# Performance work log

Measured on AMD Instinct MI355X. Metric: run time of the kernel, lower is better.

## Reference

```python
import jax, jax.numpy as jnp
import numpy as np

N_NODES = 100000
N_EDGES = 1600000
NEG_SLOPE = 0.2  # DGL GATConv default leaky_relu slope
BN_EPS = 1e-5


def setup_inputs() -> dict:
    key = jax.random.key(0)
    ks = jax.random.split(key, 10)
    feats = jax.random.normal(ks[0], (N_NODES, 128), dtype=jnp.float32)
    src = jax.random.randint(ks[1], (N_EDGES,), 0, N_NODES, dtype=jnp.int64)
    dst = jax.random.randint(ks[2], (N_EDGES,), 0, N_NODES, dtype=jnp.int64)
    fc_w = jax.random.normal(ks[3], (256, 128), dtype=jnp.float32) * 0.05   # H*D x in_feats
    attn_l = jax.random.normal(ks[4], (4, 64), dtype=jnp.float32) * 0.05
    attn_r = jax.random.normal(ks[5], (4, 64), dtype=jnp.float32) * 0.05
    res_w = jax.random.normal(ks[6], (256, 128), dtype=jnp.float32) * 0.05  # residual projection
    bias = jax.random.normal(ks[7], (4, 64), dtype=jnp.float32) * 0.05
    gamma = jnp.ones((64,), dtype=jnp.float32)
    beta = jnp.zeros((64,), dtype=jnp.float32)
    return {"feats": feats, "src": src, "dst": dst, "fc_w": fc_w,
            "attn_l": attn_l, "attn_r": attn_r, "res_w": res_w,
            "bias": bias, "gamma": gamma, "beta": beta}


def reference(feats, src, dst, fc_w, attn_l, attn_r, res_w, bias, gamma, beta):
    N = feats.shape[0]
    H, D = attn_l.shape
    # projected features [N, H, D] (feat_drop is identity in eval mode)
    h = (feats @ fc_w.T).reshape(N, H, D)
    # per-node attention logits [N, H]
    el = jnp.sum(h * attn_l[None], axis=-1)
    er = jnp.sum(h * attn_r[None], axis=-1)
    # edge logits, leaky relu
    e = el[src] + er[dst]                       # [E, H]
    e = jnp.where(e > 0, e, NEG_SLOPE * e)
    # numerically stable segment softmax over incoming edges of each dst node
    m = jax.ops.segment_max(e, dst, num_segments=N)       # [N, H]
    ex = jnp.exp(e - m[dst])                               # [E, H]
    s = jax.ops.segment_sum(ex, dst, num_segments=N)       # [N, H]
    alpha = ex / s[dst]                                    # [E, H]
    # weighted message aggregation: scatter-add alpha * h_src into dst
    msg = h[src] * alpha[:, :, None]                       # [E, H, D]
    rst = jax.ops.segment_sum(msg, dst, num_segments=N)    # [N, H, D]
    # residual projection + bias + activation (elu)
    res = (feats @ res_w.T).reshape(N, H, D)
    rst = jax.nn.elu(rst + res + bias[None])
    # mean over heads -> [N, D]
    out = rst.mean(axis=1)
    # BatchNorm1d (training stats: biased variance over the node/batch axis)
    mu = out.mean(axis=0)
    var = out.var(axis=0)
    return (out - mu) * jax.lax.rsqrt(var + BN_EPS) * gamma + beta
```

## Files before the change

### kernel.cpp

```cpp
#include <hip/hip_runtime.h>

#define N_NODES 100000
#define N_PAD   100096
#define N_EDGES 1600000
#define NEG_SLOPE 0.2f
#define BN_EPS 1e-5f

typedef __attribute__((ext_vector_type(8))) short short8;
typedef __attribute__((ext_vector_type(4))) float floatx4;

static const size_t OFF_AB   = 0;
static const size_t OFF_BB   = 25624576;
static const size_t OFF_H    = 25755648;
static const size_t OFF_RES  = 76955648;
static const size_t OFF_EL   = 128155648;
static const size_t OFF_ER   = 129755648;
static const size_t OFF_DEG  = 131355648;
static const size_t OFF_RS   = 131755648;
static const size_t OFF_CUR  = 132155664;
static const size_t OFF_ESRC = 132555664;
static const size_t OFF_BS   = 138955664;
static const size_t OFF_BN   = 138956176;

__device__ __forceinline__ unsigned short f2bf(float x) {
  unsigned int u = __float_as_uint(x);
  unsigned int r = (u + 0x7fffu + ((u >> 16) & 1u)) >> 16;
  return (unsigned short)r;
}
__device__ __forceinline__ float bf2f(unsigned short u) {
  return __uint_as_float(((unsigned int)u) << 16);
}

__global__ __launch_bounds__(256) void k_pre(
    const float* __restrict__ feats, const float* __restrict__ fc_w,
    const float* __restrict__ res_w, const int* __restrict__ dst,
    unsigned short* __restrict__ Ab, unsigned short* __restrict__ Bb,
    int* __restrict__ deg)
{
  const int b = blockIdx.x;
  if (b < 6256) {
    int c = b * 256 + threadIdx.x;
    int r = c >> 4, j = c & 15;
    unsigned short v[8];
    if (r < N_NODES) {
      const float* p = feats + (size_t)r * 128 + j * 8;
      float4 a = *(const float4*)p, bb = *(const float4*)(p + 4);
      v[0]=f2bf(a.x); v[1]=f2bf(a.y); v[2]=f2bf(a.z); v[3]=f2bf(a.w);
      v[4]=f2bf(bb.x); v[5]=f2bf(bb.y); v[6]=f2bf(bb.z); v[7]=f2bf(bb.w);
    } else {
      for (int i = 0; i < 8; i++) v[i] = 0;
    }
    size_t idx = (size_t)(r >> 7) * 2048 + ((r >> 4) & 7) * 256 + (j >> 2) * 64
               + (r & 15) + 16 * (j & 3);
    *(short8*)(Ab + idx * 8) = *(short8*)v;
  } else if (b < 12506) {
    int e = (b - 6256) * 256 + threadIdx.x;
    if (e < N_EDGES) atomicAdd(&deg[dst[e]], 1);
  } else {
    int c = (b - 12506) * 256 + threadIdx.x;
    int n = c >> 4, j = c & 15;
    const float* W = (n < 256) ? (fc_w + (size_t)n * 128) : (res_w + (size_t)(n - 256) * 128);
    const float* p = W + j * 8;
    float4 a = *(const float4*)p, bb = *(const float4*)(p + 4);
    unsigned short v[8];
    v[0]=f2bf(a.x); v[1]=f2bf(a.y); v[2]=f2bf(a.z); v[3]=f2bf(a.w);
    v[4]=f2bf(bb.x); v[5]=f2bf(bb.y); v[6]=f2bf(bb.z); v[7]=f2bf(bb.w);
    size_t idx = (size_t)(n >> 7) * 2048 + ((n >> 4) & 7) * 256 + (j >> 2) * 64
               + (n & 15) + 16 * (j & 3);
    *(short8*)(Bb + idx * 8) = *(short8*)v;
  }
}

__global__ __launch_bounds__(256) void k_mm(
    const unsigned short* __restrict__ Ab, const unsigned short* __restrict__ Bb,
    const float* __restrict__ bias, const float* __restrict__ attn_l,
    const float* __restrict__ attn_r,
    unsigned short* __restrict__ hbuf, unsigned short* __restrict__ resbuf,
    float* __restrict__ el, float* __restrict__ er)
{
  __shared__ unsigned short sA[16384];
  const int tid = threadIdx.x;
  const int w = tid >> 6, L = tid & 63;
  const int blk = blockIdx.x, nb = blockIdx.y;

  {
    const unsigned short* ga = Ab + (size_t)blk * 16384;
    #pragma unroll
    for (int i = 0; i < 8; i++) {
      int off = (i * 256 + w * 64) * 8;
      __builtin_amdgcn_global_load_lds(
          (const __attribute__((address_space(1))) unsigned int*)(ga + off + L * 8),
          (__attribute__((address_space(3))) unsigned int*)(sA + off),
          16, 0, 0);
    }
  }
  const int mh = w & 1, nh = w >> 1;
  floatx4 acc[4][4] = {};
  __syncthreads();

  const unsigned short* gb = Bb + ((size_t)nb * 2048 + nh * 4 * 256) * 8 + L * 8;
  #pragma unroll
  for (int s = 0; s < 4; s++) {
    short8 a[4], b[4];
    #pragma unroll
    for (int t = 0; t < 4; t++)
      a[t] = *(const short8*)(sA + ((mh * 4 + t) * 256 + s * 64 + L) * 8);
    #pragma unroll
    for (int t = 0; t < 4; t++)
      b[t] = *(const short8*)(gb + ((size_t)t * 256 + s * 64) * 8);
    #pragma unroll
    for (int mt = 0; mt < 4; mt++)
      #pragma unroll
      for (int nt = 0; nt < 4; nt++)
        acc[mt][nt] = __builtin_amdgcn_mfma_f32_16x16x32_bf16(a[mt], b[nt], acc[mt][nt], 0, 0, 0);
  }

  const int q = L >> 4, cn = L & 15;
  const int r0 = blk * 128 + mh * 64;
  if (nb < 2) {
    const int head = nb * 2 + nh;
    const int col0 = nb * 128 + nh * 64;
    float al[4], ar[4];
    #pragma unroll
    for (int nt = 0; nt < 4; nt++) {
      al[nt] = attn_l[head * 64 + nt * 16 + cn];
      ar[nt] = attn_r[head * 64 + nt * 16 + cn];
    }
    #pragma unroll
    for (int mt = 0; mt < 4; mt++)
      #pragma unroll
      for (int r = 0; r < 4; r++) {
        const int row = r0 + mt * 16 + q * 4 + r;
        float pl = 0.f, pr = 0.f;
        #pragma unroll
        for (int nt = 0; nt < 4; nt++) {
          pl = fmaf(acc[mt][nt][r], al[nt], pl);
          pr = fmaf(acc[mt][nt][r], ar[nt], pr);
        }
        #pragma unroll
        for (int o = 1; o < 16; o <<= 1) {
          pl += __shfl_xor(pl, o, 64);
          pr += __shfl_xor(pr, o, 64);
        }
        if (row < N_NODES) {
          #pragma unroll
          for (int nt = 0; nt < 4; nt++)
            hbuf[(size_t)row * 256 + col0 + nt * 16 + cn] = f2bf(acc[mt][nt][r]);
          if (cn == 0) {
            el[row * 4 + head] = pl;
            er[row * 4 + head] = pr;
          }
        }
      }
  } else {
    const int rc0 = (nb - 2) * 128 + nh * 64;
    #pragma unroll
    for (int mt = 0; mt < 4; mt++)
      #pragma unroll
      for (int r = 0; r < 4; r++) {
        const int row = r0 + mt * 16 + q * 4 + r;
        if (row < N_NODES)
          #pragma unroll
          for (int nt = 0; nt < 4; nt++) {
            float v = acc[mt][nt][r] + bias[rc0 + nt * 16 + cn];
            resbuf[(size_t)row * 256 + rc0 + nt * 16 + cn] = f2bf(v);
          }
      }
  }
}

__global__ __launch_bounds__(256) void k_scan1(const int* __restrict__ deg,
                                               int* __restrict__ rs, int* __restrict__ bsums)
{
  __shared__ int tmp[256];
  const int t = threadIdx.x;
  const int base = blockIdx.x * 1024 + t * 4;
  int v0 = 0, v1 = 0, v2 = 0, v3 = 0;
  if (base + 0 < N_NODES) v0 = deg[base + 0];
  if (base + 1 < N_NODES) v1 = deg[base + 1];
  if (base + 2 < N_NODES) v2 = deg[base + 2];
  if (base + 3 < N_NODES) v3 = deg[base + 3];
  const int tsum = v0 + v1 + v2 + v3;
  tmp[t] = tsum;
  __syncthreads();
  for (int o = 1; o < 256; o <<= 1) {
    int x = (t >= o) ? tmp[t - o] : 0;
    __syncthreads();
    tmp[t] += x;
    __syncthreads();
  }
  const int excl = tmp[t] - tsum;
  if (base + 0 < N_NODES) rs[base + 0] = excl;
  if (base + 1 < N_NODES) rs[base + 1] = excl + v0;
  if (base + 2 < N_NODES) rs[base + 2] = excl + v0 + v1;
  if (base + 3 < N_NODES) rs[base + 3] = excl + v0 + v1 + v2;
  if (t == 255) bsums[blockIdx.x] = tmp[t];
}

__global__ __launch_bounds__(256) void k_scan3(int* __restrict__ rs,
                                               const int* __restrict__ bsums,
                                               int* __restrict__ cursor)
{
  __shared__ int sb[128];
  const int t = threadIdx.x;
  int raw = 0;
  if (t < 128) { raw = (t < 98) ? bsums[t] : 0; sb[t] = raw; }
  __syncthreads();
  for (int o = 1; o < 128; o <<= 1) {
    int x = (t >= o && t < 128) ? sb[t - o] : 0;
    __syncthreads();
    if (t < 128) sb[t] += x;
    __syncthreads();
  }
  if (t < 128) sb[t] -= raw;
  __syncthreads();
  const int i = blockIdx.x * 256 + t;
  if (i < N_NODES) {
    int v = rs[i] + sb[i >> 10];
    rs[i] = v;
    cursor[i] = v;
  } else if (i == N_NODES) {
    rs[N_NODES] = N_EDGES;
  }
}

__global__ __launch_bounds__(256) void k_scatter(const int* __restrict__ src,
                                                 const int* __restrict__ dst,
                                                 int* __restrict__ cursor,
                                                 int* __restrict__ esrc)
{
  int e = blockIdx.x * 256 + threadIdx.x;
  if (e >= N_EDGES) return;
  int d = dst[e];
  int pos = atomicAdd(&cursor[d], 1);
  esrc[pos] = src[e];
}

__global__ __launch_bounds__(256) void k_agg(
    const unsigned short* __restrict__ hbuf, const unsigned short* __restrict__ resbuf,
    const float* __restrict__ el, const float* __restrict__ er,
    const int* __restrict__ rs, const int* __restrict__ esrc,
    float* __restrict__ out, float* __restrict__ bn)
{
  const int lane = threadIdx.x & 63;
  const int head = lane >> 4;
  const int waveG = blockIdx.x * 4 + (threadIdx.x >> 6);
  const int nW = gridDim.x * 4;
  float4 s4 = make_float4(0.f, 0.f, 0.f, 0.f);
  float4 q4 = make_float4(0.f, 0.f, 0.f, 0.f);
  for (int n = waveG; n < N_NODES; n += nW) {
    const int nu = __builtin_amdgcn_readfirstlane(n);
    const int p0 = __builtin_amdgcn_readfirstlane(rs[nu]);
    const int p1 = __builtin_amdgcn_readfirstlane(rs[nu + 1]);
    const float ern = er[nu * 4 + head];
    float4 acc = make_float4(0.f, 0.f, 0.f, 0.f);
    float ssum = 0.f;
    int p = p0;
    for (; p + 8 <= p1; p += 8) {
      int sn[8];
      #pragma unroll
      for (int i = 0; i < 8; i++) sn[i] = esrc[p + i];
      float ev[8];
      #pragma unroll
      for (int i = 0; i < 8; i++) ev[i] = el[sn[i] * 4 + head];
      ushort4 hv[8];
      #pragma unroll
      for (int i = 0; i < 8; i++)
        hv[i] = *(const ushort4*)(hbuf + (size_t)sn[i] * 256 + lane * 4);
      #pragma unroll
      for (int i = 0; i < 8; i++) {
        float e = ev[i] + ern;
        e = (e > 0.f) ? e : NEG_SLOPE * e;
        const float wgt = __expf(e);
        ssum += wgt;
        acc.x = fmaf(wgt, bf2f(hv[i].x), acc.x);
        acc.y = fmaf(wgt, bf2f(hv[i].y), acc.y);
        acc.z = fmaf(wgt, bf2f(hv[i].z), acc.z);
        acc.w = fmaf(wgt, bf2f(hv[i].w), acc.w);
      }
    }
    for (; p + 4 <= p1; p += 4) {
      int sn[4];
      #pragma unroll
      for (int i = 0; i < 4; i++) sn[i] = esrc[p + i];
      float ev[4];
      #pragma unroll
      for (int i = 0; i < 4; i++) ev[i] = el[sn[i] * 4 + head];
      ushort4 hv[4];
      #pragma unroll
      for (int i = 0; i < 4; i++)
        hv[i] = *(const ushort4*)(hbuf + (size_t)sn[i] * 256 + lane * 4);
      #pragma unroll
      for (int i = 0; i < 4; i++) {
        float e = ev[i] + ern;
        e = (e > 0.f) ? e : NEG_SLOPE * e;
        const float wgt = __expf(e);
        ssum += wgt;
        acc.x = fmaf(wgt, bf2f(hv[i].x), acc.x);
        acc.y = fmaf(wgt, bf2f(hv[i].y), acc.y);
        acc.z = fmaf(wgt, bf2f(hv[i].z), acc.z);
        acc.w = fmaf(wgt, bf2f(hv[i].w), acc.w);
      }
    }
    for (; p < p1; p++) {
      int sn = esrc[p];
      float e = el[sn * 4 + head] + ern;
      e = (e > 0.f) ? e : NEG_SLOPE * e;
      const float wgt = __expf(e);
      ssum += wgt;
      const ushort4 hv4 = *(const ushort4*)(hbuf + (size_t)sn * 256 + lane * 4);
      acc.x = fmaf(wgt, bf2f(hv4.x), acc.x);
      acc.y = fmaf(wgt, bf2f(hv4.y), acc.y);
      acc.z = fmaf(wgt, bf2f(hv4.z), acc.z);
      acc.w = fmaf(wgt, bf2f(hv4.w), acc.w);
    }
    const float inv = (p1 > p0) ? (1.0f / ssum) : 0.f;
    const ushort4 rv4 = *(const ushort4*)(resbuf + (size_t)nu * 256 + lane * 4);
    float4 v;
    v.x = fmaf(acc.x, inv, bf2f(rv4.x));
    v.y = fmaf(acc.y, inv, bf2f(rv4.y));
    v.z = fmaf(acc.z, inv, bf2f(rv4.z));
    v.w = fmaf(acc.w, inv, bf2f(rv4.w));
    v.x = (v.x > 0.f) ? v.x : (__expf(v.x) - 1.f);
    v.y = (v.y > 0.f) ? v.y : (__expf(v.y) - 1.f);
    v.z = (v.z > 0.f) ? v.z : (__expf(v.z) - 1.f);
    v.w = (v.w > 0.f) ? v.w : (__expf(v.w) - 1.f);
    v.x += __shfl_xor(v.x, 16, 64);  v.x += __shfl_xor(v.x, 32, 64);
    v.y += __shfl_xor(v.y, 16, 64);  v.y += __shfl_xor(v.y, 32, 64);
    v.z += __shfl_xor(v.z, 16, 64);  v.z += __shfl_xor(v.z, 32, 64);
    v.w += __shfl_xor(v.w, 16, 64);  v.w += __shfl_xor(v.w, 32, 64);
    if (lane < 16) {
      v.x *= 0.25f; v.y *= 0.25f; v.z *= 0.25f; v.w *= 0.25f;
      *(float4*)(out + (size_t)nu * 64 + lane * 4) = v;
      s4.x += v.x; s4.y += v.y; s4.z += v.z; s4.w += v.w;
      q4.x += v.x * v.x; q4.y += v.y * v.y; q4.z += v.z * v.z; q4.w += v.w * v.w;
    }
  }
  __shared__ float lsum[64], lsq[64];
  if (threadIdx.x < 64) { lsum[threadIdx.x] = 0.f; lsq[threadIdx.x] = 0.f; }
  __syncthreads();
  if (lane < 16) {
    atomicAdd(&lsum[lane * 4 + 0], s4.x);  atomicAdd(&lsq[lane * 4 + 0], q4.x);
    atomicAdd(&lsum[lane * 4 + 1], s4.y);  atomicAdd(&lsq[lane * 4 + 1], q4.y);
    atomicAdd(&lsum[lane * 4 + 2], s4.z);  atomicAdd(&lsq[lane * 4 + 2], q4.z);
    atomicAdd(&lsum[lane * 4 + 3], s4.w);  atomicAdd(&lsq[lane * 4 + 3], q4.w);
  }
  __syncthreads();
  if (threadIdx.x < 64) {
    atomicAdd(&bn[threadIdx.x], lsum[threadIdx.x]);
    atomicAdd(&bn[64 + threadIdx.x], lsq[threadIdx.x]);
  }
}

__global__ __launch_bounds__(256) void k_bn_apply(float* __restrict__ out,
                                                  const float* __restrict__ bn,
                                                  const float* __restrict__ gamma,
                                                  const float* __restrict__ beta)
{
  __shared__ float sc[64], sh[64];
  const int t = threadIdx.x;
  if (t < 64) {
    float mean = bn[t] * (1.0f / N_NODES);
    float var = bn[64 + t] * (1.0f / N_NODES) - mean * mean;
    float s = gamma[t] * rsqrtf(var + BN_EPS);
    sc[t] = s;
    sh[t] = beta[t] - mean * s;
  }
  __syncthreads();
  const int i = blockIdx.x * 256 + t;
  if (i >= N_NODES * 16) return;
  const int d0 = (i & 15) * 4;
  float4 v = *(float4*)(out + (size_t)i * 4);
  v.x = fmaf(v.x, sc[d0 + 0], sh[d0 + 0]);
  v.y = fmaf(v.y, sc[d0 + 1], sh[d0 + 1]);
  v.z = fmaf(v.z, sc[d0 + 2], sh[d0 + 2]);
  v.w = fmaf(v.w, sc[d0 + 3], sh[d0 + 3]);
  *(float4*)(out + (size_t)i * 4) = v;
}

extern "C" void kernel_launch(void* const* d_in, const int* in_sizes, int n_in,
                              void* d_out, int out_size, void* d_ws, size_t ws_size,
                              hipStream_t stream)
{
  const float* feats  = (const float*)d_in[0];
  const int*   src    = (const int*)d_in[1];
  const int*   dst    = (const int*)d_in[2];
  const float* fc_w   = (const float*)d_in[3];
  const float* attn_l = (const float*)d_in[4];
  const float* attn_r = (const float*)d_in[5];
  const float* res_w  = (const float*)d_in[6];
  const float* bias   = (const float*)d_in[7];
  const float* gamma  = (const float*)d_in[8];
  const float* beta   = (const float*)d_in[9];

  char* ws = (char*)d_ws;
  unsigned short* Ab     = (unsigned short*)(ws + OFF_AB);
  unsigned short* Bb     = (unsigned short*)(ws + OFF_BB);
  unsigned short* hbuf   = (unsigned short*)(ws + OFF_H);
  unsigned short* resbuf = (unsigned short*)(ws + OFF_RES);
  float* elb    = (float*)(ws + OFF_EL);
  float* erb    = (float*)(ws + OFF_ER);
  int*   deg    = (int*)(ws + OFF_DEG);
  int*   rsb    = (int*)(ws + OFF_RS);
  int*   curb   = (int*)(ws + OFF_CUR);
  int*   esrc   = (int*)(ws + OFF_ESRC);
  int*   bsums  = (int*)(ws + OFF_BS);
  float* bnb    = (float*)(ws + OFF_BN);
  float* outp   = (float*)d_out;

  hipMemsetAsync(deg, 0, N_NODES * sizeof(int), stream);
  hipMemsetAsync(bnb, 0, 128 * sizeof(float), stream);

  k_pre<<<12538, 256, 0, stream>>>(feats, fc_w, res_w, dst, Ab, Bb, deg);
  k_mm<<<dim3(782, 4), 256, 0, stream>>>(Ab, Bb, bias, attn_l, attn_r,
                                         hbuf, resbuf, elb, erb);
  k_scan1<<<98, 256, 0, stream>>>(deg, rsb, bsums);
  k_scan3<<<391, 256, 0, stream>>>(rsb, bsums, curb);
  k_scatter<<<6250, 256, 0, stream>>>(src, dst, curb, esrc);
  k_agg<<<2048, 256, 0, stream>>>(hbuf, resbuf, elb, erb, rsb, esrc, outp, bnb);
  k_bn_apply<<<6250, 256, 0, stream>>>(outp, bnb, gamma, beta);
}
```

Baseline: 532.1 us.

## Precompute edge attention weights in scatter and process two edges per wave in aggregation

```diff
diff --git a/kernel.cpp b/kernel.cpp
--- a/kernel.cpp
+++ b/kernel.cpp
@@ -21,14 +21,18 @@
 static const size_t OFF_ESRC = 132555664;
 static const size_t OFF_BS   = 138955664;
 static const size_t OFF_BN   = 138956176;
+static const size_t OFF_EW   = 138956800;
 
 __device__ __forceinline__ unsigned short f2bf(float x) {
   unsigned int u = __float_as_uint(x);
   unsigned int r = (u + 0x7fffu + ((u >> 16) & 1u)) >> 16;
   return (unsigned short)r;
 }
-__device__ __forceinline__ float bf2f(unsigned short u) {
-  return __uint_as_float(((unsigned int)u) << 16);
+__device__ __forceinline__ float bf_lo(unsigned int u) {
+  return __uint_as_float(u << 16);
+}
+__device__ __forceinline__ float bf_hi(unsigned int u) {
+  return __uint_as_float(u & 0xffff0000u);
 }
 
 __global__ __launch_bounds__(256) void k_pre(
@@ -224,131 +228,141 @@
   }
 }
 
-__global__ __launch_bounds__(256) void k_scatter(const int* __restrict__ src,
-                                                 const int* __restrict__ dst,
-                                                 int* __restrict__ cursor,
-                                                 int* __restrict__ esrc)
+__global__ __launch_bounds__(256) void k_scatter(
+    const int* __restrict__ src, const int* __restrict__ dst,
+    const float* __restrict__ el, const float* __restrict__ er,
+    int* __restrict__ cursor, int* __restrict__ esrc, float* __restrict__ ewgt)
 {
   int e = blockIdx.x * 256 + threadIdx.x;
   if (e >= N_EDGES) return;
-  int d = dst[e];
-  int pos = atomicAdd(&cursor[d], 1);
-  esrc[pos] = src[e];
+  const int s = src[e], d = dst[e];
+  const float4 l4 = *(const float4*)(el + (size_t)s * 4);
+  const float4 r4 = *(const float4*)(er + (size_t)d * 4);
+  float4 w;
+  float t;
+  t = l4.x + r4.x; t = (t > 0.f) ? t : NEG_SLOPE * t; w.x = __expf(t);
+  t = l4.y + r4.y; t = (t > 0.f) ? t : NEG_SLOPE * t; w.y = __expf(t);
+  t = l4.z + r4.z; t = (t > 0.f) ? t : NEG_SLOPE * t; w.z = __expf(t);
+  t = l4.w + r4.w; t = (t > 0.f) ? t : NEG_SLOPE * t; w.w = __expf(t);
+  const int pos = atomicAdd(&cursor[d], 1);
+  esrc[pos] = s;
+  *(float4*)(ewgt + (size_t)pos * 4) = w;
 }
 
 __global__ __launch_bounds__(256) void k_agg(
     const unsigned short* __restrict__ hbuf, const unsigned short* __restrict__ resbuf,
-    const float* __restrict__ el, const float* __restrict__ er,
     const int* __restrict__ rs, const int* __restrict__ esrc,
+    const float* __restrict__ ewgt,
     float* __restrict__ out, float* __restrict__ bn)
 {
-  const int lane = threadIdx.x & 63;
-  const int head = lane >> 4;
-  const int waveG = blockIdx.x * 4 + (threadIdx.x >> 6);
+  const int tid = threadIdx.x;
+  const int L = tid & 63;
+  const int half = L >> 5;
+  const int j = L & 31;
+  const int head = j >> 3;
+  const int c = j & 7;
+  const int waveG = blockIdx.x * 4 + (tid >> 6);
   const int nW = gridDim.x * 4;
-  float4 s4 = make_float4(0.f, 0.f, 0.f, 0.f);
-  float4 q4 = make_float4(0.f, 0.f, 0.f, 0.f);
+
+  float s8[8], q8[8];
+  #pragma unroll
+  for (int i = 0; i < 8; i++) { s8[i] = 0.f; q8[i] = 0.f; }
+
   for (int n = waveG; n < N_NODES; n += nW) {
     const int nu = __builtin_amdgcn_readfirstlane(n);
     const int p0 = __builtin_amdgcn_readfirstlane(rs[nu]);
     const int p1 = __builtin_amdgcn_readfirstlane(rs[nu + 1]);
-    const float ern = er[nu * 4 + head];
-    float4 acc = make_float4(0.f, 0.f, 0.f, 0.f);
+    float acc[8];
+    #pragma unroll
+    for (int i = 0; i < 8; i++) acc[i] = 0.f;
     float ssum = 0.f;
-    int p = p0;
-    for (; p + 8 <= p1; p += 8) {
-      int sn[8];
-      #pragma unroll
-      for (int i = 0; i < 8; i++) sn[i] = esrc[p + i];
-      float ev[8];
-      #pragma unroll
-      for (int i = 0; i < 8; i++) ev[i] = el[sn[i] * 4 + head];
-      ushort4 hv[8];
-      #pragma unroll
-      for (int i = 0; i < 8; i++)
-        hv[i] = *(const ushort4*)(hbuf + (size_t)sn[i] * 256 + lane * 4);
+
+    if (p0 < p1) {
+      float w0, w1;
+      uint4 h0, h1;
+      #define LOAD_SLOT(W, H, PP) {                                            \
+        int pe = (PP) + half;                                                  \
+        bool valid = pe < p1;                                                  \
+        int pec = valid ? pe : p0;                                             \
+        float wr = ewgt[(size_t)pec * 4 + head];                               \
+        int sn = esrc[pec];                                                    \
+        W = valid ? wr : 0.f;                                                  \
+        H = *(const uint4*)(hbuf + (size_t)sn * 256 + j * 8);                  \
+      }
+      #define CONSUME(W, H) {                                                  \
+        ssum += W;                                                             \
+        acc[0] = fmaf(W, bf_lo(H.x), acc[0]);                                  \
+        acc[1] = fmaf(W, bf_hi(H.x), acc[1]);                                  \
+        acc[2] = fmaf(W, bf_lo(H.y), acc[2]);                                  \
+        acc[3] = fmaf(W, bf_hi(H.y), acc[3]);                                  \
+        acc[4] = fmaf(W, bf_lo(H.z), acc[4]);                                  \
+        acc[5] = fmaf(W, bf_hi(H.z), acc[5]);                                  \
+        acc[6] = fmaf(W, bf_lo(H.w), acc[6]);                                  \
+        acc[7] = fmaf(W, bf_hi(H.w), acc[7]);                                  \
+      }
+      LOAD_SLOT(w0, h0, p0)
+      LOAD_SLOT(w1, h1, p0 + 2)
+      for (int p = p0; p < p1; p += 4) {
+        CONSUME(w0, h0)
+        LOAD_SLOT(w0, h0, p + 4)
+        CONSUME(w1, h1)
+        LOAD_SLOT(w1, h1, p + 6)
+      }
+      #undef LOAD_SLOT
+      #undef CONSUME
+    }
+
+    #pragma unroll
+    for (int i = 0; i < 8; i++) acc[i] += __shfl_xor(acc[i], 32, 64);
+    ssum += __shfl_xor(ssum, 32, 64);
+    const float inv = (p1 > p0) ? (1.0f / ssum) : 0.f;
+
+    const uint4 rv = *(const uint4*)(resbuf + (size_t)nu * 256 + j * 8);
+    float v[8];
+    v[0] = fmaf(acc[0], inv, bf_lo(rv.x));
+    v[1] = fmaf(acc[1], inv, bf_hi(rv.x));
+    v[2] = fmaf(acc[2], inv, bf_lo(rv.y));
+    v[3] = fmaf(acc[3], inv, bf_hi(rv.y));
+    v[4] = fmaf(acc[4], inv, bf_lo(rv.z));
+    v[5] = fmaf(acc[5], inv, bf_hi(rv.z));
+    v[6] = fmaf(acc[6], inv, bf_lo(rv.w));
+    v[7] = fmaf(acc[7], inv, bf_hi(rv.w));
+    #pragma unroll
+    for (int i = 0; i < 8; i++)
+      v[i] = (v[i] > 0.f) ? v[i] : (__expf(v[i]) - 1.f);
+
+    #pragma unroll
+    for (int i = 0; i < 8; i++) {
+      v[i] += __shfl_xor(v[i], 8, 64);
+      v[i] += __shfl_xor(v[i], 16, 64);
+      v[i] *= 0.25f;
+    }
+
+    if (L < 8) {
+      *(float4*)(out + (size_t)nu * 64 + c * 8)     = make_float4(v[0], v[1], v[2], v[3]);
+      *(float4*)(out + (size_t)nu * 64 + c * 8 + 4) = make_float4(v[4], v[5], v[6], v[7]);
       #pragma unroll
       for (int i = 0; i < 8; i++) {
-        float e = ev[i] + ern;
-        e = (e > 0.f) ? e : NEG_SLOPE * e;
-        const float wgt = __expf(e);
-        ssum += wgt;
-        acc.x = fmaf(wgt, bf2f(hv[i].x), acc.x);
-        acc.y = fmaf(wgt, bf2f(hv[i].y), acc.y);
-        acc.z = fmaf(wgt, bf2f(hv[i].z), acc.z);
-        acc.w = fmaf(wgt, bf2f(hv[i].w), acc.w);
-      }
-    }
-    for (; p + 4 <= p1; p += 4) {
-      int sn[4];
-      #pragma unroll
-      for (int i = 0; i < 4; i++) sn[i] = esrc[p + i];
-      float ev[4];
-      #pragma unroll
-      for (int i = 0; i < 4; i++) ev[i] = el[sn[i] * 4 + head];
-      ushort4 hv[4];
-      #pragma unroll
-      for (int i = 0; i < 4; i++)
-        hv[i] = *(const ushort4*)(hbuf + (size_t)sn[i] * 256 + lane * 4);
-      #pragma unroll
-      for (int i = 0; i < 4; i++) {
-        float e = ev[i] + ern;
-        e = (e > 0.f) ? e : NEG_SLOPE * e;
-        const float wgt = __expf(e);
-        ssum += wgt;
-        acc.x = fmaf(wgt, bf2f(hv[i].x), acc.x);
-        acc.y = fmaf(wgt, bf2f(hv[i].y), acc.y);
-        acc.z = fmaf(wgt, bf2f(hv[i].z), acc.z);
-        acc.w = fmaf(wgt, bf2f(hv[i].w), acc.w);
-      }
-    }
-    for (; p < p1; p++) {
-      int sn = esrc[p];
-      float e = el[sn * 4 + head] + ern;
-      e = (e > 0.f) ? e : NEG_SLOPE * e;
-      const float wgt = __expf(e);
-      ssum += wgt;
-      const ushort4 hv4 = *(const ushort4*)(hbuf + (size_t)sn * 256 + lane * 4);
-      acc.x = fmaf(wgt, bf2f(hv4.x), acc.x);
-      acc.y = fmaf(wgt, bf2f(hv4.y), acc.y);
-      acc.z = fmaf(wgt, bf2f(hv4.z), acc.z);
-      acc.w = fmaf(wgt, bf2f(hv4.w), acc.w);
-    }
-    const float inv = (p1 > p0) ? (1.0f / ssum) : 0.f;
-    const ushort4 rv4 = *(const ushort4*)(resbuf + (size_t)nu * 256 + lane * 4);
-    float4 v;
-    v.x = fmaf(acc.x, inv, bf2f(rv4.x));
-    v.y = fmaf(acc.y, inv, bf2f(rv4.y));
-    v.z = fmaf(acc.z, inv, bf2f(rv4.z));
-    v.w = fmaf(acc.w, inv, bf2f(rv4.w));
-    v.x = (v.x > 0.f) ? v.x : (__expf(v.x) - 1.f);
-    v.y = (v.y > 0.f) ? v.y : (__expf(v.y) - 1.f);
-    v.z = (v.z > 0.f) ? v.z : (__expf(v.z) - 1.f);
-    v.w = (v.w > 0.f) ? v.w : (__expf(v.w) - 1.f);
-    v.x += __shfl_xor(v.x, 16, 64);  v.x += __shfl_xor(v.x, 32, 64);
-    v.y += __shfl_xor(v.y, 16, 64);  v.y += __shfl_xor(v.y, 32, 64);
-    v.z += __shfl_xor(v.z, 16, 64);  v.z += __shfl_xor(v.z, 32, 64);
-    v.w += __shfl_xor(v.w, 16, 64);  v.w += __shfl_xor(v.w, 32, 64);
-    if (lane < 16) {
-      v.x *= 0.25f; v.y *= 0.25f; v.z *= 0.25f; v.w *= 0.25f;
-      *(float4*)(out + (size_t)nu * 64 + lane * 4) = v;
-      s4.x += v.x; s4.y += v.y; s4.z += v.z; s4.w += v.w;
-      q4.x += v.x * v.x; q4.y += v.y * v.y; q4.z += v.z * v.z; q4.w += v.w * v.w;
-    }
-  }
+        s8[i] += v[i];
+        q8[i] += v[i] * v[i];
+      }
+    }
+  }
+
   __shared__ float lsum[64], lsq[64];
-  if (threadIdx.x < 64) { lsum[threadIdx.x] = 0.f; lsq[threadIdx.x] = 0.f; }
-  __syncthreads();
-  if (lane < 16) {
-    atomicAdd(&lsum[lane * 4 + 0], s4.x);  atomicAdd(&lsq[lane * 4 + 0], q4.x);
-    atomicAdd(&lsum[lane * 4 + 1], s4.y);  atomicAdd(&lsq[lane * 4 + 1], q4.y);
-    atomicAdd(&lsum[lane * 4 + 2], s4.z);  atomicAdd(&lsq[lane * 4 + 2], q4.z);
-    atomicAdd(&lsum[lane * 4 + 3], s4.w);  atomicAdd(&lsq[lane * 4 + 3], q4.w);
-  }
-  __syncthreads();
-  if (threadIdx.x < 64) {
-    atomicAdd(&bn[threadIdx.x], lsum[threadIdx.x]);
-    atomicAdd(&bn[64 + threadIdx.x], lsq[threadIdx.x]);
+  if (tid < 64) { lsum[tid] = 0.f; lsq[tid] = 0.f; }
+  __syncthreads();
+  if (L < 8) {
+    #pragma unroll
+    for (int i = 0; i < 8; i++) {
+      atomicAdd(&lsum[c * 8 + i], s8[i]);
+      atomicAdd(&lsq[c * 8 + i], q8[i]);
+    }
+  }
+  __syncthreads();
+  if (tid < 64) {
+    atomicAdd(&bn[tid], lsum[tid]);
+    atomicAdd(&bn[64 + tid], lsq[tid]);
   }
 }
 
@@ -406,6 +420,7 @@
   int*   esrc   = (int*)(ws + OFF_ESRC);
   int*   bsums  = (int*)(ws + OFF_BS);
   float* bnb    = (float*)(ws + OFF_BN);
+  float* ewgt   = (float*)(ws + OFF_EW);
   float* outp   = (float*)d_out;
 
   hipMemsetAsync(deg, 0, N_NODES * sizeof(int), stream);
@@ -416,7 +431,7 @@
                                          hbuf, resbuf, elb, erb);
   k_scan1<<<98, 256, 0, stream>>>(deg, rsb, bsums);
   k_scan3<<<391, 256, 0, stream>>>(rsb, bsums, curb);
-  k_scatter<<<6250, 256, 0, stream>>>(src, dst, curb, esrc);
-  k_agg<<<2048, 256, 0, stream>>>(hbuf, resbuf, elb, erb, rsb, esrc, outp, bnb);
+  k_scatter<<<6250, 256, 0, stream>>>(src, dst, elb, erb, curb, esrc, ewgt);
+  k_agg<<<2048, 256, 0, stream>>>(hbuf, resbuf, rsb, esrc, ewgt, outp, bnb);
   k_bn_apply<<<6250, 256, 0, stream>>>(outp, bnb, gamma, beta);
 }
```

Result: slower. 547.2 us (+2.8%).

## Transpose MFMA operands for packed bf16 stores and add nontemporal hints

Applied to the files above, without the earlier changes.

```diff
diff --git a/kernel.cpp b/kernel.cpp
--- a/kernel.cpp
+++ b/kernel.cpp
@@ -8,6 +8,8 @@
 
 typedef __attribute__((ext_vector_type(8))) short short8;
 typedef __attribute__((ext_vector_type(4))) float floatx4;
+typedef __attribute__((ext_vector_type(4))) float fx4;
+typedef __attribute__((ext_vector_type(2))) unsigned int ux2;
 
 static const size_t OFF_AB   = 0;
 static const size_t OFF_BB   = 25624576;
@@ -30,6 +32,15 @@
 __device__ __forceinline__ float bf2f(unsigned short u) {
   return __uint_as_float(((unsigned int)u) << 16);
 }
+__device__ __forceinline__ float bf_lo(unsigned int u) {
+  return __uint_as_float(u << 16);
+}
+__device__ __forceinline__ float bf_hi(unsigned int u) {
+  return __uint_as_float(u & 0xffff0000u);
+}
+__device__ __forceinline__ unsigned int pack2bf(float a, float b) {
+  return (unsigned int)f2bf(a) | ((unsigned int)f2bf(b) << 16);
+}
 
 __global__ __launch_bounds__(256) void k_pre(
     const float* __restrict__ feats, const float* __restrict__ fc_w,
@@ -44,9 +55,10 @@
     unsigned short v[8];
     if (r < N_NODES) {
       const float* p = feats + (size_t)r * 128 + j * 8;
-      float4 a = *(const float4*)p, bb = *(const float4*)(p + 4);
-      v[0]=f2bf(a.x); v[1]=f2bf(a.y); v[2]=f2bf(a.z); v[3]=f2bf(a.w);
-      v[4]=f2bf(bb.x); v[5]=f2bf(bb.y); v[6]=f2bf(bb.z); v[7]=f2bf(bb.w);
+      fx4 a  = __builtin_nontemporal_load((const fx4*)p);
+      fx4 bb = __builtin_nontemporal_load((const fx4*)(p + 4));
+      v[0]=f2bf(a[0]); v[1]=f2bf(a[1]); v[2]=f2bf(a[2]); v[3]=f2bf(a[3]);
+      v[4]=f2bf(bb[0]); v[5]=f2bf(bb[1]); v[6]=f2bf(bb[2]); v[7]=f2bf(bb[3]);
     } else {
       for (int i = 0; i < 8; i++) v[i] = 0;
     }
@@ -55,7 +67,7 @@
     *(short8*)(Ab + idx * 8) = *(short8*)v;
   } else if (b < 12506) {
     int e = (b - 6256) * 256 + threadIdx.x;
-    if (e < N_EDGES) atomicAdd(&deg[dst[e]], 1);
+    if (e < N_EDGES) atomicAdd(&deg[__builtin_nontemporal_load(dst + e)], 1);
   } else {
     int c = (b - 12506) * 256 + threadIdx.x;
     int n = c >> 4, j = c & 15;
@@ -112,7 +124,7 @@
     for (int mt = 0; mt < 4; mt++)
       #pragma unroll
       for (int nt = 0; nt < 4; nt++)
-        acc[mt][nt] = __builtin_amdgcn_mfma_f32_16x16x32_bf16(a[mt], b[nt], acc[mt][nt], 0, 0, 0);
+        acc[mt][nt] = __builtin_amdgcn_mfma_f32_16x16x32_bf16(b[nt], a[mt], acc[mt][nt], 0, 0, 0);
   }
 
   const int q = L >> 4, cn = L & 15;
@@ -120,52 +132,58 @@
   if (nb < 2) {
     const int head = nb * 2 + nh;
     const int col0 = nb * 128 + nh * 64;
-    float al[4], ar[4];
+    float4 alv[4], arv[4];
     #pragma unroll
     for (int nt = 0; nt < 4; nt++) {
-      al[nt] = attn_l[head * 64 + nt * 16 + cn];
-      ar[nt] = attn_r[head * 64 + nt * 16 + cn];
-    }
-    #pragma unroll
-    for (int mt = 0; mt < 4; mt++)
-      #pragma unroll
-      for (int r = 0; r < 4; r++) {
-        const int row = r0 + mt * 16 + q * 4 + r;
-        float pl = 0.f, pr = 0.f;
+      alv[nt] = *(const float4*)(attn_l + head * 64 + nt * 16 + q * 4);
+      arv[nt] = *(const float4*)(attn_r + head * 64 + nt * 16 + q * 4);
+    }
+    #pragma unroll
+    for (int mt = 0; mt < 4; mt++) {
+      const int row = r0 + mt * 16 + cn;
+      float pl = 0.f, pr = 0.f;
+      #pragma unroll
+      for (int nt = 0; nt < 4; nt++) {
+        pl = fmaf(acc[mt][nt][0], alv[nt].x, pl); pr = fmaf(acc[mt][nt][0], arv[nt].x, pr);
+        pl = fmaf(acc[mt][nt][1], alv[nt].y, pl); pr = fmaf(acc[mt][nt][1], arv[nt].y, pr);
+        pl = fmaf(acc[mt][nt][2], alv[nt].z, pl); pr = fmaf(acc[mt][nt][2], arv[nt].z, pr);
+        pl = fmaf(acc[mt][nt][3], alv[nt].w, pl); pr = fmaf(acc[mt][nt][3], arv[nt].w, pr);
+      }
+      pl += __shfl_xor(pl, 16, 64);  pl += __shfl_xor(pl, 32, 64);
+      pr += __shfl_xor(pr, 16, 64);  pr += __shfl_xor(pr, 32, 64);
+      if (row < N_NODES) {
         #pragma unroll
         for (int nt = 0; nt < 4; nt++) {
-          pl = fmaf(acc[mt][nt][r], al[nt], pl);
-          pr = fmaf(acc[mt][nt][r], ar[nt], pr);
+          ux2 pk;
+          pk[0] = pack2bf(acc[mt][nt][0], acc[mt][nt][1]);
+          pk[1] = pack2bf(acc[mt][nt][2], acc[mt][nt][3]);
+          *(ux2*)(hbuf + (size_t)row * 256 + col0 + nt * 16 + q * 4) = pk;
         }
-        #pragma unroll
-        for (int o = 1; o < 16; o <<= 1) {
-          pl += __shfl_xor(pl, o, 64);
-          pr += __shfl_xor(pr, o, 64);
-        }
-        if (row < N_NODES) {
-          #pragma unroll
-          for (int nt = 0; nt < 4; nt++)
-            hbuf[(size_t)row * 256 + col0 + nt * 16 + cn] = f2bf(acc[mt][nt][r]);
-          if (cn == 0) {
-            el[row * 4 + head] = pl;
-            er[row * 4 + head] = pr;
-          }
+        if (q == 0) {
+          el[row * 4 + head] = pl;
+          er[row * 4 + head] = pr;
         }
       }
+    }
   } else {
     const int rc0 = (nb - 2) * 128 + nh * 64;
-    #pragma unroll
-    for (int mt = 0; mt < 4; mt++)
-      #pragma unroll
-      for (int r = 0; r < 4; r++) {
-        const int row = r0 + mt * 16 + q * 4 + r;
-        if (row < N_NODES)
-          #pragma unroll
-          for (int nt = 0; nt < 4; nt++) {
-            float v = acc[mt][nt][r] + bias[rc0 + nt * 16 + cn];
-            resbuf[(size_t)row * 256 + rc0 + nt * 16 + cn] = f2bf(v);
-          }
+    float4 bv[4];
+    #pragma unroll
+    for (int nt = 0; nt < 4; nt++)
+      bv[nt] = *(const float4*)(bias + rc0 + nt * 16 + q * 4);
+    #pragma unroll
+    for (int mt = 0; mt < 4; mt++) {
+      const int row = r0 + mt * 16 + cn;
+      if (row < N_NODES) {
+        #pragma unroll
+        for (int nt = 0; nt < 4; nt++) {
+          ux2 pk;
+          pk[0] = pack2bf(acc[mt][nt][0] + bv[nt].x, acc[mt][nt][1] + bv[nt].y);
+          pk[1] = pack2bf(acc[mt][nt][2] + bv[nt].z, acc[mt][nt][3] + bv[nt].w);
+          __builtin_nontemporal_store(pk, (ux2*)(resbuf + (size_t)row * 256 + rc0 + nt * 16 + q * 4));
+        }
       }
+    }
   }
 }
 
@@ -231,9 +249,10 @@
 {
   int e = blockIdx.x * 256 + threadIdx.x;
   if (e >= N_EDGES) return;
-  int d = dst[e];
+  int s = __builtin_nontemporal_load(src + e);
+  int d = __builtin_nontemporal_load(dst + e);
   int pos = atomicAdd(&cursor[d], 1);
-  esrc[pos] = src[e];
+  esrc[pos] = s;
 }
 
 __global__ __launch_bounds__(256) void k_agg(
@@ -315,12 +334,12 @@
       acc.w = fmaf(wgt, bf2f(hv4.w), acc.w);
     }
     const float inv = (p1 > p0) ? (1.0f / ssum) : 0.f;
-    const ushort4 rv4 = *(const ushort4*)(resbuf + (size_t)nu * 256 + lane * 4);
+    const ux2 rv = __builtin_nontemporal_load((const ux2*)(resbuf + (size_t)nu * 256 + lane * 4));
     float4 v;
-    v.x = fmaf(acc.x, inv, bf2f(rv4.x));
-    v.y = fmaf(acc.y, inv, bf2f(rv4.y));
-    v.z = fmaf(acc.z, inv, bf2f(rv4.z));
-    v.w = fmaf(acc.w, inv, bf2f(rv4.w));
+    v.x = fmaf(acc.x, inv, bf_lo(rv[0]));
+    v.y = fmaf(acc.y, inv, bf_hi(rv[0]));
+    v.z = fmaf(acc.z, inv, bf_lo(rv[1]));
+    v.w = fmaf(acc.w, inv, bf_hi(rv[1]));
     v.x = (v.x > 0.f) ? v.x : (__expf(v.x) - 1.f);
     v.y = (v.y > 0.f) ? v.y : (__expf(v.y) - 1.f);
     v.z = (v.z > 0.f) ? v.z : (__expf(v.z) - 1.f);
@@ -331,7 +350,8 @@
     v.w += __shfl_xor(v.w, 16, 64);  v.w += __shfl_xor(v.w, 32, 64);
     if (lane < 16) {
       v.x *= 0.25f; v.y *= 0.25f; v.z *= 0.25f; v.w *= 0.25f;
-      *(float4*)(out + (size_t)nu * 64 + lane * 4) = v;
+      fx4 vv; vv[0] = v.x; vv[1] = v.y; vv[2] = v.z; vv[3] = v.w;
+      __builtin_nontemporal_store(vv, (fx4*)(out + (size_t)nu * 64 + lane * 4));
       s4.x += v.x; s4.y += v.y; s4.z += v.z; s4.w += v.w;
       q4.x += v.x * v.x; q4.y += v.y * v.y; q4.z += v.z * v.z; q4.w += v.w * v.w;
     }
```

Result: slower. 553.6 us (+4.0%).
